# Performance work log

Hardware: AMD Instinct MI355X
Metric: run time of the kernel (lower is better)

Reference implementation:

```python
import jax, jax.numpy as jnp
import numpy as np

N_HEADS = 32
N_KV = 8
HEAD_DIM = 128
ROPE_THETA = 10000.0
PAST_LEN = 2048


def _rope_cos_sin(position_ids):
    # inv_freq: [head_dim/2]
    inv_freq = 1.0 / (ROPE_THETA ** (jnp.arange(0, HEAD_DIM, 2, dtype=jnp.float32) / HEAD_DIM))
    freqs = position_ids.astype(jnp.float32)[..., None] * inv_freq  # [B, S, hd/2]
    emb = jnp.concatenate([freqs, freqs], axis=-1)  # [B, S, hd]
    return jnp.cos(emb), jnp.sin(emb)


def _rotate_half(x):
    x1, x2 = jnp.split(x, 2, axis=-1)
    return jnp.concatenate([-x2, x1], axis=-1)


def setup_inputs() -> dict:
    key = jax.random.key(0)
    ks = jax.random.split(key, 10)
    B, S = 1, 2048
    IN = 8192
    s = 0.02
    return {
        "hidden_states": jax.random.normal(ks[0], (B, S, IN), jnp.float32),
        "position_ids": (jnp.arange(S, dtype=jnp.int32) + PAST_LEN)[None, :],
        "cache_k": jax.random.normal(ks[1], (B, N_KV, PAST_LEN, HEAD_DIM), jnp.float32),
        "cache_v": jax.random.normal(ks[2], (B, N_KV, PAST_LEN, HEAD_DIM), jnp.float32),
        "Wq": jax.random.normal(ks[3], (N_HEADS * HEAD_DIM, IN), jnp.float32) * s,
        "bq": jax.random.normal(ks[4], (N_HEADS * HEAD_DIM,), jnp.float32) * s,
        "Wk": jax.random.normal(ks[5], (N_KV * HEAD_DIM, IN), jnp.float32) * s,
        "bk": jax.random.normal(ks[6], (N_KV * HEAD_DIM,), jnp.float32) * s,
        "Wv": jax.random.normal(ks[7], (N_KV * HEAD_DIM, IN), jnp.float32) * s,
        "bv": jax.random.normal(ks[8], (N_KV * HEAD_DIM,), jnp.float32) * s,
        "Wo": jax.random.normal(ks[9], (N_HEADS * HEAD_DIM, N_HEADS * HEAD_DIM), jnp.float32) * s,
    }


def reference(hidden_states, position_ids, cache_k, cache_v, Wq, bq, Wk, bk, Wv, bv, Wo):
    B, Sq, _ = hidden_states.shape
    G = N_HEADS // N_KV

    # QKV projections -> [B, H, S, D]
    q = (hidden_states @ Wq.T + bq).reshape(B, Sq, N_HEADS, HEAD_DIM).transpose(0, 2, 1, 3)
    k = (hidden_states @ Wk.T + bk).reshape(B, Sq, N_KV, HEAD_DIM).transpose(0, 2, 1, 3)
    v = (hidden_states @ Wv.T + bv).reshape(B, Sq, N_KV, HEAD_DIM).transpose(0, 2, 1, 3)

    # RoPE
    cos, sin = _rope_cos_sin(position_ids)  # [B, Sq, D]
    cos, sin = cos[:, None], sin[:, None]   # broadcast over heads
    q = q * cos + _rotate_half(q) * sin
    k = k * cos + _rotate_half(k) * sin

    # KV cache concat
    key = jnp.concatenate([cache_k, k], axis=2)   # [B, Kv, Sk, D]
    value = jnp.concatenate([cache_v, v], axis=2)
    Sk = key.shape[2]
    past_len = Sk - Sq

    # GQA attention (grouped einsum == repeat_interleave + SDPA)
    qg = q.reshape(B, N_KV, G, Sq, HEAD_DIM)
    scale = 1.0 / jnp.sqrt(jnp.float32(HEAD_DIM))
    scores = jnp.einsum("bkgqd,bkld->bkgql", qg, key) * scale  # [B, Kv, G, Sq, Sk]

    q_pos = past_len + jnp.arange(Sq)
    mask = jnp.arange(Sk)[None, :] <= q_pos[:, None]  # [Sq, Sk]
    scores = jnp.where(mask[None, None, None], scores, -jnp.inf)
    attn = jax.nn.softmax(scores, axis=-1)

    ctx = jnp.einsum("bkgql,bkld->bkgqd", attn, value)
    ctx = ctx.reshape(B, N_HEADS, Sq, HEAD_DIM).transpose(0, 2, 1, 3).reshape(B, Sq, N_HEADS * HEAD_DIM)
    out = ctx @ Wo.T
    return out, key, value
```

## Files before the change

kernel.cpp:

```cpp
#include <hip/hip_runtime.h>
#include <hip/hip_bf16.h>
#include <math.h>

typedef float f32x4 __attribute__((ext_vector_type(4)));
typedef short s16x8 __attribute__((ext_vector_type(8)));
typedef __bf16 bf16x8 __attribute__((ext_vector_type(8)));

__device__ __forceinline__ unsigned short f2bf(float f) {
  return __builtin_bit_cast(unsigned short, (__bf16)f);
}

__device__ __forceinline__ f32x4 mfma16(s16x8 a, s16x8 b, f32x4 c) {
  return __builtin_amdgcn_mfma_f32_16x16x32_bf16(
      __builtin_bit_cast(bf16x8, a), __builtin_bit_cast(bf16x8, b), c, 0, 0, 0);
}

#define GLDS(gp, lp) __builtin_amdgcn_global_load_lds(                      \
    (__attribute__((address_space(1))) void*)(gp),                          \
    (__attribute__((address_space(3))) void*)(lp), 16, 0, 0)

struct __attribute__((aligned(8))) us4 { unsigned short x, y, z, w; };
__device__ __forceinline__ us4 cvt4(float4 v) {
  us4 r; r.x = f2bf(v.x); r.y = f2bf(v.y); r.z = f2bf(v.z); r.w = f2bf(v.w);
  return r;
}

__global__ __launch_bounds__(256) void conv_all(
    const float4* __restrict__ h, const float4* __restrict__ wq,
    const float4* __restrict__ wk, const float4* __restrict__ wv,
    const float4* __restrict__ wo, const float4* __restrict__ bq,
    const float4* __restrict__ bk, const float4* __restrict__ bv,
    us4* __restrict__ hbf, us4* __restrict__ wqkvbf, us4* __restrict__ wobf,
    float4* __restrict__ biasc)
{
  const unsigned int U = 20973056u;
  const unsigned int stride = gridDim.x * blockDim.x;
  for (unsigned int u = blockIdx.x * blockDim.x + threadIdx.x; u < U; u += stride) {
    if (u < 4194304u) {
      hbf[u] = cvt4(h[u]);
    } else if (u < 12582912u) {
      unsigned int o = u - 4194304u;  wqkvbf[o] = cvt4(wq[o]);
    } else if (u < 14680064u) {
      unsigned int o = u - 12582912u; wqkvbf[8388608u + o] = cvt4(wk[o]);
    } else if (u < 16777216u) {
      unsigned int o = u - 14680064u; wqkvbf[10485760u + o] = cvt4(wv[o]);
    } else if (u < 20971520u) {
      unsigned int o = u - 16777216u; wobf[o] = cvt4(wo[o]);
    } else {
      unsigned int o = u - 20971520u;
      float4 v = (o < 1024u) ? bq[o] : (o < 1280u) ? bk[o - 1024u] : bv[o - 1280u];
      biasc[o] = v;
    }
  }
}

__global__ __launch_bounds__(256) void rope_table(const int* __restrict__ pos_ids,
                                                  float* __restrict__ cost,
                                                  float* __restrict__ sint)
{
  int idx = blockIdx.x * blockDim.x + threadIdx.x;
  if (idx >= 131072) return;
  int s = idx >> 6, i = idx & 63;
  double invf = exp(-((double)i / 64.0) * 9.210340371976184);
  double ang = (double)pos_ids[s] * invf;
  cost[idx] = (float)cos(ang);
  sint[idx] = (float)sin(ang);
}

template<int NF>
__global__ __launch_bounds__(512, 2) void gemm8p(const unsigned short* __restrict__ A,
                                                 const unsigned short* __restrict__ B,
                                                 const float* __restrict__ bias,
                                                 float* __restrict__ C,
                                                 int M, int N, int K)
{
  constexpr int BN = NF * 64;
  constexpr int BUFSZ = 32768 + BN * 128;
  __shared__ char smem[2 * BUFSZ];
  const int tid = threadIdx.x;
  const int l = tid & 63;
  const int w = tid >> 6;
  const int wm = w >> 2, wn = w & 3;
  const int wr = wm * 128;
  const int wc = wn * (16 * NF);
  const int lk16 = (l >> 4) * 16;

  const int nwg = gridDim.x;
  const int s = (blockIdx.x & 7) * (nwg >> 3) + (blockIdx.x >> 3);
  const int NBY = M >> 8;
  const int by = s % NBY, bx = s / NBY;
  const size_t arow0 = (size_t)by * 256;
  const size_t brow0 = (size_t)bx * BN;
  const size_t Kb = (size_t)K * 2;
  const char* Ab = (const char*)A;
  const char* Bb = (const char*)B;

  f32x4 acc[8][NF];
#pragma unroll
  for (int i = 0; i < 8; ++i)
#pragma unroll
    for (int j = 0; j < NF; ++j) acc[i][j] = (f32x4){0.f, 0.f, 0.f, 0.f};

  auto STAGE = [&](int t, char* buf) {
    const size_t k0b = (size_t)t * 128;
#pragma unroll
    for (int cc = 0; cc < 4; ++cc) {
      const int ch = cc * 512 + tid;
      const int r = ch >> 3;
      const int c2s = ((ch & 7) * 16) ^ ((r & 7) << 4);
      GLDS(Ab + (arow0 + r) * Kb + k0b + c2s, buf + ch * 16);
    }
#pragma unroll
    for (int cc = 0; cc < NF; ++cc) {
      const int ch = cc * 512 + tid;
      const int r = ch >> 3;
      const int c2s = ((ch & 7) * 16) ^ ((r & 7) << 4);
      GLDS(Bb + (brow0 + r) * Kb + k0b + c2s, buf + 32768 + ch * 16);
    }
  };

  const int nt = K >> 6;
  STAGE(0, smem);
  asm volatile("s_waitcnt vmcnt(0)" ::: "memory");
  __builtin_amdgcn_s_barrier();

  for (int t = 0; t < nt; ++t) {
    char* cur = smem + (t & 1) * BUFSZ;
    if (t + 1 < nt) STAGE(t + 1, smem + ((t + 1) & 1) * BUFSZ);
    s16x8 bfr[NF][2];
#pragma unroll
    for (int n = 0; n < NF; ++n)
#pragma unroll
      for (int k = 0; k < 2; ++k) {
        const int r = wc + n * 16 + (l & 15);
        const int c2 = k * 64 + lk16;
        bfr[n][k] = *(const s16x8*)(cur + 32768 + (r * 128 + (c2 ^ ((r & 7) << 4))));
      }
#pragma unroll
    for (int qd = 0; qd < 4; ++qd) {
      s16x8 afr[2][2];
#pragma unroll
      for (int i = 0; i < 2; ++i)
#pragma unroll
        for (int k = 0; k < 2; ++k) {
          const int r = wr + (qd * 2 + i) * 16 + (l & 15);
          const int c2 = k * 64 + lk16;
          afr[i][k] = *(const s16x8*)(cur + (r * 128 + (c2 ^ ((r & 7) << 4))));
        }
      __builtin_amdgcn_s_setprio(1);
#pragma unroll
      for (int i = 0; i < 2; ++i)
#pragma unroll
        for (int n = 0; n < NF; ++n)
#pragma unroll
          for (int k = 0; k < 2; ++k)
            acc[qd * 2 + i][n] = mfma16(afr[i][k], bfr[n][k], acc[qd * 2 + i][n]);
      __builtin_amdgcn_s_setprio(0);
    }
    asm volatile("s_waitcnt vmcnt(0)" ::: "memory");
    __builtin_amdgcn_s_barrier();
  }

  const int r0 = (int)arow0 + wr + (l >> 4) * 4;
  const int c0 = (int)brow0 + wc + (l & 15);
#pragma unroll
  for (int mi = 0; mi < 8; ++mi) {
#pragma unroll
    for (int ni = 0; ni < NF; ++ni) {
      const int c = c0 + ni * 16;
      const float bvv = bias ? bias[c] : 0.f;
#pragma unroll
      for (int rr = 0; rr < 4; ++rr) {
        const int r = r0 + mi * 16 + rr;
        C[(size_t)r * N + c] = acc[mi][ni][rr] + bvv;
      }
    }
  }
}

__global__ __launch_bounds__(256) void rope_scatter(
    const float* __restrict__ qkv, const float* __restrict__ cost,
    const float* __restrict__ sint, const float* __restrict__ cache_k,
    const float* __restrict__ cache_v, float* __restrict__ keyout,
    float* __restrict__ valout, unsigned short* __restrict__ qbf,
    char* __restrict__ kswz, char* __restrict__ vswz)
{
  const float rs = 0.08838834764831845f;
  const int stride = gridDim.x * blockDim.x;
  for (int idx = blockIdx.x * blockDim.x + threadIdx.x; idx < 11534336; idx += stride) {
    if (idx < 4194304) {
      int i = idx & 63, hh = (idx >> 6) & 31, s = idx >> 11;
      const float* base = qkv + (size_t)s * 6144 + hh * 128 + i;
      float q1 = base[0], q2 = base[64];
      float c = cost[s * 64 + i], sn = sint[s * 64 + i];
      float o1 = (q1 * c - q2 * sn) * rs, o2 = (q2 * c + q1 * sn) * rs;
      unsigned short* qd = qbf + ((size_t)hh * 2048 + s) * 128 + i;
      qd[0] = f2bf(o1); qd[64] = f2bf(o2);
    } else if (idx < 5242880) {
      int j = idx - 4194304;
      int i = j & 63, kh = (j >> 6) & 7, s = j >> 9;
      const float* base = qkv + (size_t)s * 6144 + 4096 + kh * 128 + i;
      float k1 = base[0], k2 = base[64];
      float c = cost[s * 64 + i], sn = sint[s * 64 + i];
      float o1 = k1 * c - k2 * sn, o2 = k2 * c + k1 * sn;
      float* kd = keyout + ((size_t)kh * 4096 + 2048 + s) * 128 + i;
      kd[0] = o1; kd[64] = o2;
      int t = 32 + (s >> 6), r = s & 63;
      char* tb = kswz + (size_t)(kh * 64 + t) * 16384;
      *(unsigned short*)(tb + ((r * 256 + i * 2) ^ ((r & 7) << 4))) = f2bf(o1);
      *(unsigned short*)(tb + ((r * 256 + (i + 64) * 2) ^ ((r & 7) << 4))) = f2bf(o2);
    } else if (idx < 7340032) {
      int j = idx - 5242880;
      int d = j & 127, kh = (j >> 7) & 7, s = j >> 10;
      float v = qkv[(size_t)s * 6144 + 5120 + kh * 128 + d];
      valout[((size_t)kh * 4096 + 2048 + s) * 128 + d] = v;
      int t = 32 + (s >> 6), c = s & 63;
      char* tb = vswz + (size_t)(kh * 64 + t) * 16384;
      *(unsigned short*)(tb + ((d * 128 + c * 2) ^ ((d & 7) << 4))) = f2bf(v);
    } else if (idx < 9437184) {
      int j = idx - 7340032;
      int d = j & 127, s = (j >> 7) & 2047, kh = j >> 18;
      float v = cache_k[(size_t)(kh * 2048 + s) * 128 + d];
      keyout[((size_t)kh * 4096 + s) * 128 + d] = v;
      int t = s >> 6, r = s & 63;
      char* tb = kswz + (size_t)(kh * 64 + t) * 16384;
      *(unsigned short*)(tb + ((r * 256 + d * 2) ^ ((r & 7) << 4))) = f2bf(v);
    } else {
      int j = idx - 9437184;
      int d = j & 127, s = (j >> 7) & 2047, kh = j >> 18;
      float v = cache_v[(size_t)(kh * 2048 + s) * 128 + d];
      valout[((size_t)kh * 4096 + s) * 128 + d] = v;
      int t = s >> 6, c = s & 63;
      char* tb = vswz + (size_t)(kh * 64 + t) * 16384;
      *(unsigned short*)(tb + ((d * 128 + c * 2) ^ ((d & 7) << 4))) = f2bf(v);
    }
  }
}

__global__ __launch_bounds__(512) void attn_fwd(const unsigned short* __restrict__ qbf,
                                                const char* __restrict__ kswz,
                                                const char* __restrict__ vswz,
                                                unsigned short* __restrict__ ctx)
{
  __shared__ char smem[81920];
  char* Ps = smem + 65536;
  const int tid = threadIdx.x;
  const int l = tid & 63;
  const int w = tid >> 6;
  const int d = blockIdx.x;
  const int b = d >> 5;
  const int qt = (b < 8) ? b : 23 - b;
  const int h = (d & 7) * 4 + ((d >> 3) & 3);
  const int kh = h >> 2;
  const int nt = 2 * qt + 34;
  const int qrow16 = (l >> 4) * 4;
  const float L2E = 1.44269504f;
  const float M16 = 23.0831098f;

  s16x8 aq[4];
  {
    const int qr = qt * 128 + w * 16 + (l & 15);
    const unsigned short* qp = qbf + ((size_t)h * 2048 + qr) * 128 + (l >> 4) * 8;
#pragma unroll
    for (int kc = 0; kc < 4; ++kc) aq[kc] = *(const s16x8*)(qp + kc * 32);
  }
  f32x4 o[8];
#pragma unroll
  for (int i = 0; i < 8; ++i) o[i] = (f32x4){0.f, 0.f, 0.f, 0.f};
  float ls[4] = {0.f, 0.f, 0.f, 0.f};

  const char* kb0 = kswz + (size_t)kh * (64 * 16384);
  const char* vb0 = vswz + (size_t)kh * (64 * 16384);
  char* Pw = Ps + w * 2048;

  auto STAGE = [&](int t, int c) {
    const char* kb = kb0 + (size_t)t * 16384;
    const char* vb = vb0 + (size_t)t * 16384;
    char* Kt = smem + c * 32768;
    char* Vt = Kt + 16384;
#pragma unroll
    for (int j = 0; j < 2; ++j) {
      const int cw = j * 8 + w;
      GLDS(kb + (cw * 64 + l) * 16, Kt + cw * 1024);
      GLDS(vb + (cw * 64 + l) * 16, Vt + cw * 1024);
    }
  };

  STAGE(0, 0);
  int c = 0;
  for (int t = 0; t < nt; ++t) {
    asm volatile("s_waitcnt vmcnt(0)" ::: "memory");
    __builtin_amdgcn_s_barrier();
    asm volatile("" ::: "memory");
    if (t + 1 < nt) STAGE(t + 1, c ^ 1);
    const char* Kt = smem + c * 32768;
    const char* Vt = Kt + 16384;

    f32x4 s[4];
#pragma unroll
    for (int i = 0; i < 4; ++i) s[i] = (f32x4){0.f, 0.f, 0.f, 0.f};
    __builtin_amdgcn_s_setprio(1);
#pragma unroll
    for (int kc = 0; kc < 4; ++kc) {
      const int d0b = (kc * 32 + (l >> 4) * 8) * 2;
#pragma unroll
      for (int ni = 0; ni < 4; ++ni) {
        const int row = ni * 16 + (l & 15);
        s16x8 kf = *(const s16x8*)(Kt + ((row * 256 + d0b) ^ ((row & 7) << 4)));
        s[ni] = mfma16(aq[kc], kf, s[ni]);
      }
    }
    __builtin_amdgcn_s_setprio(0);
    if (t >= nt - 2) {
      const int qpos_b = 2048 + qt * 128 + w * 16 + qrow16;
      const int kvcol = (l & 15);
#pragma unroll
      for (int ni = 0; ni < 4; ++ni) {
        const int kvpos = t * 64 + ni * 16 + kvcol;
#pragma unroll
        for (int rr = 0; rr < 4; ++rr)
          if (kvpos > qpos_b + rr) s[ni][rr] = -1e30f;
      }
    }
#pragma unroll
    for (int ni = 0; ni < 4; ++ni) {
      const int colb = (ni * 16 + (l & 15)) * 2;
#pragma unroll
      for (int rr = 0; rr < 4; ++rr) {
        const float p = __builtin_amdgcn_exp2f(__builtin_fmaf(s[ni][rr], L2E, -M16));
        ls[rr] += p;
        const int q = qrow16 + rr;
        *(__bf16*)(Pw + ((q * 128 + colb) ^ ((q & 7) << 4))) = (__bf16)p;
      }
    }
    s16x8 pa[2];
#pragma unroll
    for (int kc2 = 0; kc2 < 2; ++kc2) {
      const int q = l & 15;
      const int kvb = (kc2 * 32 + (l >> 4) * 8) * 2;
      pa[kc2] = *(const s16x8*)(Pw + ((q * 128 + kvb) ^ ((q & 7) << 4)));
    }
    __builtin_amdgcn_s_setprio(1);
#pragma unroll
    for (int sub = 0; sub < 8; ++sub) {
      const int dd = sub * 16 + (l & 15);
#pragma unroll
      for (int kc2 = 0; kc2 < 2; ++kc2) {
        const int kvb = (kc2 * 32 + (l >> 4) * 8) * 2;
        s16x8 vf = *(const s16x8*)(Vt + ((dd * 128 + kvb) ^ ((dd & 7) << 4)));
        o[sub] = mfma16(pa[kc2], vf, o[sub]);
      }
    }
    __builtin_amdgcn_s_setprio(0);
    asm volatile("" ::: "memory");
    c ^= 1;
  }

#pragma unroll
  for (int rr = 0; rr < 4; ++rr) {
    float v = ls[rr];
    v += __shfl_xor(v, 1);
    v += __shfl_xor(v, 2);
    v += __shfl_xor(v, 4);
    v += __shfl_xor(v, 8);
    ls[rr] = 1.0f / v;
  }
  const int r0 = qt * 128 + w * 16 + qrow16;
  const int c0 = h * 128 + (l & 15);
#pragma unroll
  for (int sub = 0; sub < 8; ++sub)
#pragma unroll
    for (int rr = 0; rr < 4; ++rr) {
      const float v = o[sub][rr] * ls[rr];
      ctx[(size_t)(r0 + rr) * 4096 + c0 + sub * 16] = f2bf(v);
    }
}

extern "C" void kernel_launch(void* const* d_in, const int* in_sizes, int n_in,
                              void* d_out, int out_size, void* d_ws, size_t ws_size,
                              hipStream_t stream) {
  (void)in_sizes; (void)n_in; (void)out_size; (void)ws_size;
  const float* hs     = (const float*)d_in[0];
  const int*   pos    = (const int*)d_in[1];
  const float* cachek = (const float*)d_in[2];
  const float* cachev = (const float*)d_in[3];
  const float* Wq     = (const float*)d_in[4];
  const float* bq     = (const float*)d_in[5];
  const float* Wk     = (const float*)d_in[6];
  const float* bk     = (const float*)d_in[7];
  const float* Wv     = (const float*)d_in[8];
  const float* bv     = (const float*)d_in[9];
  const float* Wo     = (const float*)d_in[10];

  float* out    = (float*)d_out;
  float* keyout = out + (size_t)2048 * 4096;
  float* valout = keyout + (size_t)8 * 4096 * 128;

  char* ws = (char*)d_ws;
  unsigned short* hbf    = (unsigned short*)(ws + 0);
  unsigned short* qbf    = (unsigned short*)(ws + 0);
  char*           kswz   = ws + 16777216;
  char*           vswz   = ws + 25165824;
  unsigned short* wqkvbf = (unsigned short*)(ws + 33554432);
  unsigned short* wobf   = (unsigned short*)(ws + 134217728);
  float*          qkvf   = (float*)(ws + 167772160);
  unsigned short* ctxbf  = (unsigned short*)(ws + 167772160);
  float*          cost   = (float*)(ws + 218103808);
  float*          sint   = (float*)(ws + 218628096);
  float*          biasc  = (float*)(ws + 219152384);

  conv_all<<<2048, 256, 0, stream>>>((const float4*)hs, (const float4*)Wq,
                                     (const float4*)Wk, (const float4*)Wv,
                                     (const float4*)Wo, (const float4*)bq,
                                     (const float4*)bk, (const float4*)bv,
                                     (us4*)hbf, (us4*)wqkvbf, (us4*)wobf,
                                     (float4*)biasc);
  rope_table<<<512, 256, 0, stream>>>(pos, cost, sint);
  gemm8p<3><<<256, 512, 0, stream>>>(hbf, wqkvbf, biasc, qkvf, 2048, 6144, 8192);
  rope_scatter<<<2048, 256, 0, stream>>>(qkvf, cost, sint, cachek, cachev,
                                         keyout, valout, qbf, kswz, vswz);
  attn_fwd<<<512, 512, 0, stream>>>(qbf, kswz, vswz, ctxbf);
  gemm8p<2><<<256, 512, 0, stream>>>(ctxbf, wobf, nullptr, out, 2048, 4096, 4096);
}
```

Before: 558.9 us.

## Fuse fp32 weight-to-bf16 conversion into GEMM B-tile staging

Drops the separate conversion pass over Wq/Wk/Wv/Wo. The GEMM now loads fp32 weight rows straight into registers, converts them to bf16 and writes them into swizzled LDS, choosing among the three QKV weight pointers by row range. This removes a full read of the weights plus a bf16 write and read-back. In exchange the GEMM reads twice as many bytes for B, and the register-staged loads and LDS writes replace the async global_load_lds path, which adds register pressure and serialises the stores before the barrier.

New measurement: 559.5 us. Within noise of the previous version (+0.1%).

```diff
diff --git a/kernel.cpp b/kernel.cpp
--- a/kernel.cpp
+++ b/kernel.cpp
@@ -4,6 +4,7 @@
 
 typedef float f32x4 __attribute__((ext_vector_type(4)));
 typedef short s16x8 __attribute__((ext_vector_type(8)));
+typedef unsigned short u16x8 __attribute__((ext_vector_type(8)));
 typedef __bf16 bf16x8 __attribute__((ext_vector_type(8)));
 
 __device__ __forceinline__ unsigned short f2bf(float f) {
@@ -24,30 +25,25 @@
   us4 r; r.x = f2bf(v.x); r.y = f2bf(v.y); r.z = f2bf(v.z); r.w = f2bf(v.w);
   return r;
 }
+__device__ __forceinline__ u16x8 cvt8(float4 a, float4 b) {
+  u16x8 r;
+  r[0] = f2bf(a.x); r[1] = f2bf(a.y); r[2] = f2bf(a.z); r[3] = f2bf(a.w);
+  r[4] = f2bf(b.x); r[5] = f2bf(b.y); r[6] = f2bf(b.z); r[7] = f2bf(b.w);
+  return r;
+}
 
 __global__ __launch_bounds__(256) void conv_all(
-    const float4* __restrict__ h, const float4* __restrict__ wq,
-    const float4* __restrict__ wk, const float4* __restrict__ wv,
-    const float4* __restrict__ wo, const float4* __restrict__ bq,
+    const float4* __restrict__ h, const float4* __restrict__ bq,
     const float4* __restrict__ bk, const float4* __restrict__ bv,
-    us4* __restrict__ hbf, us4* __restrict__ wqkvbf, us4* __restrict__ wobf,
-    float4* __restrict__ biasc)
+    us4* __restrict__ hbf, float4* __restrict__ biasc)
 {
-  const unsigned int U = 20973056u;
+  const unsigned int U = 4195840u;
   const unsigned int stride = gridDim.x * blockDim.x;
   for (unsigned int u = blockIdx.x * blockDim.x + threadIdx.x; u < U; u += stride) {
     if (u < 4194304u) {
       hbf[u] = cvt4(h[u]);
-    } else if (u < 12582912u) {
-      unsigned int o = u - 4194304u;  wqkvbf[o] = cvt4(wq[o]);
-    } else if (u < 14680064u) {
-      unsigned int o = u - 12582912u; wqkvbf[8388608u + o] = cvt4(wk[o]);
-    } else if (u < 16777216u) {
-      unsigned int o = u - 14680064u; wqkvbf[10485760u + o] = cvt4(wv[o]);
-    } else if (u < 20971520u) {
-      unsigned int o = u - 16777216u; wobf[o] = cvt4(wo[o]);
     } else {
-      unsigned int o = u - 20971520u;
+      unsigned int o = u - 4194304u;
       float4 v = (o < 1024u) ? bq[o] : (o < 1280u) ? bk[o - 1024u] : bv[o - 1280u];
       biasc[o] = v;
     }
@@ -68,11 +64,14 @@
 }
 
 template<int NF>
-__global__ __launch_bounds__(512, 2) void gemm8p(const unsigned short* __restrict__ A,
-                                                 const unsigned short* __restrict__ B,
-                                                 const float* __restrict__ bias,
-                                                 float* __restrict__ C,
-                                                 int M, int N, int K)
+__global__ __launch_bounds__(512, 2) void gemm_wf(const unsigned short* __restrict__ A,
+                                                  const float* __restrict__ B0,
+                                                  const float* __restrict__ B1,
+                                                  const float* __restrict__ B2,
+                                                  int r1, int r2,
+                                                  const float* __restrict__ bias,
+                                                  float* __restrict__ C,
+                                                  int M, int N, int K)
 {
   constexpr int BN = NF * 64;
   constexpr int BUFSZ = 32768 + BN * 128;
@@ -90,10 +89,9 @@
   const int NBY = M >> 8;
   const int by = s % NBY, bx = s / NBY;
   const size_t arow0 = (size_t)by * 256;
-  const size_t brow0 = (size_t)bx * BN;
+  const int brow0 = bx * BN;
   const size_t Kb = (size_t)K * 2;
   const char* Ab = (const char*)A;
-  const char* Bb = (const char*)B;
 
   f32x4 acc[8][NF];
 #pragma unroll
@@ -101,7 +99,9 @@
 #pragma unroll
     for (int j = 0; j < NF; ++j) acc[i][j] = (f32x4){0.f, 0.f, 0.f, 0.f};
 
-  auto STAGE = [&](int t, char* buf) {
+  float4 breg[NF][2];
+
+  auto STAGE_A = [&](int t, char* buf) {
     const size_t k0b = (size_t)t * 128;
 #pragma unroll
     for (int cc = 0; cc < 4; ++cc) {
@@ -110,23 +110,44 @@
       const int c2s = ((ch & 7) * 16) ^ ((r & 7) << 4);
       GLDS(Ab + (arow0 + r) * Kb + k0b + c2s, buf + ch * 16);
     }
+  };
+  auto B_LOAD = [&](int t) {
 #pragma unroll
     for (int cc = 0; cc < NF; ++cc) {
       const int ch = cc * 512 + tid;
       const int r = ch >> 3;
-      const int c2s = ((ch & 7) * 16) ^ ((r & 7) << 4);
-      GLDS(Bb + (brow0 + r) * Kb + k0b + c2s, buf + 32768 + ch * 16);
+      const int rg = brow0 + r;
+      const float* bp; int rl;
+      if (rg < r1)      { bp = B0; rl = rg; }
+      else if (rg < r2) { bp = B1; rl = rg - r1; }
+      else              { bp = B2; rl = rg - r2; }
+      const float* p = bp + (size_t)rl * K + t * 64 + (ch & 7) * 8;
+      breg[cc][0] = *(const float4*)p;
+      breg[cc][1] = *(const float4*)(p + 4);
     }
   };
+  auto B_WRITE = [&](char* buf) {
+#pragma unroll
+    for (int cc = 0; cc < NF; ++cc) {
+      const int ch = cc * 512 + tid;
+      const int r = ch >> 3;
+      const int off = ((ch & 7) * 16) ^ ((r & 7) << 4);
+      *(u16x8*)(buf + 32768 + r * 128 + off) = cvt8(breg[cc][0], breg[cc][1]);
+    }
+  };
 
   const int nt = K >> 6;
-  STAGE(0, smem);
+  STAGE_A(0, smem);
+  B_LOAD(0);
   asm volatile("s_waitcnt vmcnt(0)" ::: "memory");
+  B_WRITE(smem);
+  asm volatile("s_waitcnt lgkmcnt(0)" ::: "memory");
   __builtin_amdgcn_s_barrier();
 
   for (int t = 0; t < nt; ++t) {
     char* cur = smem + (t & 1) * BUFSZ;
-    if (t + 1 < nt) STAGE(t + 1, smem + ((t + 1) & 1) * BUFSZ);
+    char* nxt = smem + ((t + 1) & 1) * BUFSZ;
+    if (t + 1 < nt) { STAGE_A(t + 1, nxt); B_LOAD(t + 1); }
     s16x8 bfr[NF][2];
 #pragma unroll
     for (int n = 0; n < NF; ++n)
@@ -158,11 +179,13 @@
       __builtin_amdgcn_s_setprio(0);
     }
     asm volatile("s_waitcnt vmcnt(0)" ::: "memory");
+    if (t + 1 < nt) B_WRITE(nxt);
+    asm volatile("s_waitcnt lgkmcnt(0)" ::: "memory");
     __builtin_amdgcn_s_barrier();
   }
 
   const int r0 = (int)arow0 + wr + (l >> 4) * 4;
-  const int c0 = (int)brow0 + wc + (l & 15);
+  const int c0 = brow0 + wc + (l & 15);
 #pragma unroll
   for (int mi = 0; mi < 8; ++mi) {
 #pragma unroll
@@ -401,24 +424,21 @@
   unsigned short* qbf    = (unsigned short*)(ws + 0);
   char*           kswz   = ws + 16777216;
   char*           vswz   = ws + 25165824;
-  unsigned short* wqkvbf = (unsigned short*)(ws + 33554432);
-  unsigned short* wobf   = (unsigned short*)(ws + 134217728);
   float*          qkvf   = (float*)(ws + 167772160);
   unsigned short* ctxbf  = (unsigned short*)(ws + 167772160);
   float*          cost   = (float*)(ws + 218103808);
   float*          sint   = (float*)(ws + 218628096);
   float*          biasc  = (float*)(ws + 219152384);
 
-  conv_all<<<2048, 256, 0, stream>>>((const float4*)hs, (const float4*)Wq,
-                                     (const float4*)Wk, (const float4*)Wv,
-                                     (const float4*)Wo, (const float4*)bq,
+  conv_all<<<2048, 256, 0, stream>>>((const float4*)hs, (const float4*)bq,
                                      (const float4*)bk, (const float4*)bv,
-                                     (us4*)hbf, (us4*)wqkvbf, (us4*)wobf,
-                                     (float4*)biasc);
+                                     (us4*)hbf, (float4*)biasc);
   rope_table<<<512, 256, 0, stream>>>(pos, cost, sint);
-  gemm8p<3><<<256, 512, 0, stream>>>(hbf, wqkvbf, biasc, qkvf, 2048, 6144, 8192);
+  gemm_wf<3><<<256, 512, 0, stream>>>(hbf, Wq, Wk, Wv, 4096, 5120, biasc, qkvf,
+                                      2048, 6144, 8192);
   rope_scatter<<<2048, 256, 0, stream>>>(qkvf, cost, sint, cachek, cachev,
                                          keyout, valout, qbf, kswz, vswz);
   attn_fwd<<<512, 512, 0, stream>>>(qbf, kswz, vswz, ctxbf);
-  gemm8p<2><<<256, 512, 0, stream>>>(ctxbf, wobf, nullptr, out, 2048, 4096, 4096);
-}
+  gemm_wf<2><<<256, 512, 0, stream>>>(ctxbf, Wo, Wo, Wo, 1 << 30, 1 << 30, nullptr,
+                                      out, 2048, 4096, 4096);
+}
```
